# Kernel optimization log

Measured on AMD Instinct MI355X. Metric: run time of the kernel, lower is better.

Reference implementation:

```python
import jax, jax.numpy as jnp
import numpy as np

B, S, D, H = 2, 2048, 512, 8
DK = D // H

def setup_inputs() -> dict:
    key = jax.random.key(0)
    ks = jax.random.split(key, 13)
    inp = {
        'query': jax.random.normal(ks[0], (B, S, D), jnp.float32),
        'key': jax.random.normal(ks[1], (B, S, D), jnp.float32),
        'value': jax.random.normal(ks[2], (B, S, D), jnp.float32),
        'group_prob': jax.random.uniform(ks[3], (B, S, S), jnp.float32),
        'mask': jax.random.randint(ks[4], (B, S, S), 0, 2, jnp.int32),
        'Wq': jax.random.normal(ks[5], (D, D), jnp.float32) * 0.02,
        'bq': jax.random.normal(ks[6], (D,), jnp.float32) * 0.02,
        'Wk': jax.random.normal(ks[7], (D, D), jnp.float32) * 0.02,
        'bk': jax.random.normal(ks[8], (D,), jnp.float32) * 0.02,
        'Wv': jax.random.normal(ks[9], (D, D), jnp.float32) * 0.02,
        'bv': jax.random.normal(ks[10], (D,), jnp.float32) * 0.02,
        'Wo': jax.random.normal(ks[11], (D, D), jnp.float32) * 0.02,
        'bo': jax.random.normal(ks[12], (D,), jnp.float32) * 0.02,
    }
    return inp

def reference(query, key, value, group_prob, mask, Wq, bq, Wk, bk, Wv, bv, Wo, bo):
    # project and split heads: [B,S,D] -> [B,H,S,dk]
    def proj(x, W, b):
        return (x @ W.T + b).reshape(B, S, H, DK).transpose(0, 2, 1, 3)
    q = proj(query, Wq, bq)
    k = proj(key, Wk, bk)
    v = proj(value, Wv, bv)
    scale = 1.0 / np.sqrt(DK).astype(np.float32)
    scores = jnp.einsum('bhqd,bhkd->bhqk', q, k) * scale  # [B,H,S,S]
    # allowed = mask | identity-diagonal; disallowed positions get -1e9
    diag = jnp.eye(S, dtype=bool)
    allowed = (mask.astype(bool) | diag)[:, None, :, :]  # [B,1,S,S]
    scores = jnp.where(allowed, scores, jnp.float32(-1e9))
    p_attn = jax.nn.softmax(scores, axis=-1) * group_prob[:, None, :, :]
    # dropout is identity in eval/deterministic mode
    x = jnp.einsum('bhqk,bhkd->bhqd', p_attn, v)  # [B,H,S,dk]
    x = x.transpose(0, 2, 1, 3).reshape(B, S, D)
    return x @ Wo.T + bo
```

## Files before the change

### kernel.cpp

```cpp
#include <hip/hip_runtime.h>
#include <hip/hip_bf16.h>
#include <cstdint>
#include <cstddef>

typedef __attribute__((ext_vector_type(8))) short bf16x8;
typedef __attribute__((ext_vector_type(4))) float f32x4;
typedef __attribute__((address_space(3))) void lds_void;
typedef const __attribute__((address_space(1))) void g_void;

constexpr int Bc = 2, Sc = 2048, Dc = 512, Hc = 8, DKc = 64;
constexpr int SPLIT = 2;
constexpr int NKT = Sc / 64;
constexpr int KT_PER = NKT / SPLIT;
constexpr float CSC = 0.18033688011112042f;

struct alignas(16) us8 { unsigned short u[8]; };
struct alignas(8) us4 { unsigned short u[4]; };

__device__ __forceinline__ unsigned short f2bf(float x) {
  union { float f; unsigned int u; } v; v.f = x;
  unsigned int r = (v.u + 0x7FFFu + ((v.u >> 16) & 1u)) >> 16;
  return (unsigned short)r;
}

__device__ __forceinline__ float bf2f(unsigned short u) {
  union { unsigned int u; float f; } v; v.u = ((unsigned int)u) << 16;
  return v.f;
}

__device__ __forceinline__ us8 cvt8(float4 a, float4 b) {
  us8 o;
  o.u[0] = f2bf(a.x); o.u[1] = f2bf(a.y); o.u[2] = f2bf(a.z); o.u[3] = f2bf(a.w);
  o.u[4] = f2bf(b.x); o.u[5] = f2bf(b.y); o.u[6] = f2bf(b.z); o.u[7] = f2bf(b.w);
  return o;
}

struct PArgs {
  const float* g; const int* m; unsigned short* gp;
  const float* wsrc[4]; unsigned short* wdst[4];
};

__global__ __launch_bounds__(256)
void prepass(PArgs pa)
{
  const int bx = blockIdx.x;
  const int tid = threadIdx.x;
  if (bx < 2048) {
    const int idx = bx;
    const int b = idx >> 10, rest = idx & 1023, qt = rest >> 5, kt = rest & 31;
    const int colb = tid & 15, hi = (tid >> 4) & 3, wid = tid >> 6;
    const int q = qt * 64 + wid * 16 + colb;
    const int k0 = kt * 64 + hi * 4;
    const float* grow = pa.g + ((size_t)b * Sc + q) * Sc + k0;
    const int* mrow = pa.m + ((size_t)b * Sc + q) * Sc + k0;
    unsigned short vals[16];
#pragma unroll
    for (int n = 0; n < 4; ++n) {
      float4 gv = *(const float4*)(grow + n * 16);
      int4 mv = *(const int4*)(mrow + n * 16);
      const int kb = k0 + n * 16;
      const float gg[4] = {gv.x, gv.y, gv.z, gv.w};
      const int mm[4] = {mv.x, mv.y, mv.z, mv.w};
#pragma unroll
      for (int rr = 0; rr < 4; ++rr) {
        const bool allowed = (mm[rr] != 0) || (kb + rr == q);
        vals[n * 4 + rr] = allowed ? (unsigned short)(f2bf(gg[rr]) | 1u) : (unsigned short)0;
      }
    }
    us8* o = (us8*)(pa.gp + (((size_t)idx * 256) + tid) * 16);
    o[0] = *(us8*)&vals[0];
    o[1] = *(us8*)&vals[8];
  } else {
    const int r = bx - 2048;
    const int wi = r >> 3, sub = r & 7;
    const float* s = pa.wsrc[wi];
    unsigned short* d = pa.wdst[wi];
#pragma unroll
    for (int t = 0; t < 16; ++t) {
      const int i = sub * 4096 + t * 256 + tid;
      float4 a = ((const float4*)s)[(size_t)i * 2];
      float4 b = ((const float4*)s)[(size_t)i * 2 + 1];
      ((us8*)d)[i] = cvt8(a, b);
    }
  }
}

struct GArgs {
  const void* A[3];
  const unsigned short* W[3];
  const float* bias[3];
  void* C[3];
  int mode[3];
  float osc[3];
};

template<int A_FP32>
__global__ __launch_bounds__(256)
void gemm_bn64(GArgs ga)
{
  __shared__ unsigned short As[128][64];
  __shared__ unsigned short Bs[64][64];

  constexpr int K = 512, N = 512;
  const int z = blockIdx.z;
  const unsigned short* Wp = ga.W[z];
  const float* bias = ga.bias[z];
  const int mode = ga.mode[z];
  const float osc = ga.osc[z];

  const int tid = threadIdx.x, lane = tid & 63, w = tid >> 6;
  const int m0 = blockIdx.x * 128, n0 = blockIdx.y * 64;
  const int wm = w >> 1, wn = w & 1;
  const int colb = lane & 15, hi = lane >> 4, rowb = hi * 4;
  const int swz = (colb & 7) << 4;

  f32x4 acc[4][2];
#pragma unroll
  for (int i = 0; i < 4; ++i)
#pragma unroll
    for (int j = 0; j < 2; ++j) acc[i][j] = (f32x4){0.f, 0.f, 0.f, 0.f};

  const int lrow8 = lane >> 3;
  const int cb = ((lane & 7) * 16) ^ (lrow8 << 4);

  for (int k0 = 0; k0 < K; k0 += 64) {
    if (k0) __syncthreads();
#pragma unroll
    for (int i = 0; i < 2; ++i) {
      const int u = w + i * 4;
      const int row = u * 8 + lrow8;
      const unsigned short* bsrc = Wp + (size_t)(n0 + row) * K + k0 + (cb >> 1);
      __builtin_amdgcn_global_load_lds((g_void*)bsrc, (lds_void*)((char*)&Bs[0][0] + u * 1024), 16, 0, 0);
    }
    if (A_FP32) {
      const float* Af = (const float*)ga.A[z];
#pragma unroll
      for (int i = 0; i < 4; ++i) {
        const int u = w * 4 + i;
        const int row = u * 8 + lrow8;
        const float* src = Af + (size_t)(m0 + row) * K + k0 + (cb >> 1);
        float4 v0 = *(const float4*)src, v1 = *(const float4*)(src + 4);
        *(us8*)((char*)&As[0][0] + u * 1024 + lane * 16) = cvt8(v0, v1);
      }
    } else {
      const unsigned short* Ab = (const unsigned short*)ga.A[z];
#pragma unroll
      for (int i = 0; i < 4; ++i) {
        const int u = w * 4 + i;
        const int row = u * 8 + lrow8;
        const unsigned short* asrc = Ab + (size_t)(m0 + row) * K + k0 + (cb >> 1);
        __builtin_amdgcn_global_load_lds((g_void*)asrc, (lds_void*)((char*)&As[0][0] + u * 1024), 16, 0, 0);
      }
    }
    asm volatile("s_waitcnt vmcnt(0)" ::: "memory");
    __syncthreads();

    char* ab = (char*)&As[0][0];
    char* bb = (char*)&Bs[0][0];
#pragma unroll
    for (int kk = 0; kk < 2; ++kk) {
      bf16x8 af[4], bfr[2];
#pragma unroll
      for (int mf = 0; mf < 4; ++mf) {
        const int ar = wm * 64 + mf * 16 + colb;
        af[mf] = *(const bf16x8*)(ab + ar * 128 + ((kk * 64 + hi * 16) ^ swz));
      }
#pragma unroll
      for (int nf = 0; nf < 2; ++nf) {
        const int br = wn * 32 + nf * 16 + colb;
        bfr[nf] = *(const bf16x8*)(bb + br * 128 + ((kk * 64 + hi * 16) ^ swz));
      }
      __builtin_amdgcn_s_setprio(1);
#pragma unroll
      for (int mf = 0; mf < 4; ++mf)
#pragma unroll
        for (int nf = 0; nf < 2; ++nf)
          acc[mf][nf] = __builtin_amdgcn_mfma_f32_16x16x32_bf16(af[mf], bfr[nf], acc[mf][nf], 0, 0, 0);
      __builtin_amdgcn_s_setprio(0);
    }
  }

#pragma unroll
  for (int nf = 0; nf < 2; ++nf) {
    const int gn = n0 + wn * 32 + nf * 16 + colb;
    const float bv = bias[gn];
    if (mode == 1) {
      unsigned short* Cp = (unsigned short*)ga.C[z];
#pragma unroll
      for (int mf = 0; mf < 4; ++mf) {
        const int gm = m0 + wm * 64 + mf * 16 + rowb;
        const int bb_ = gm >> 11, ss = gm & (Sc - 1);
        us4 vv;
#pragma unroll
        for (int rr = 0; rr < 4; ++rr) vv.u[rr] = f2bf(acc[mf][nf][rr] + bv);
        *(us4*)(Cp + ((size_t)bb_ * N + gn) * Sc + ss) = vv;
      }
    } else if (mode == 0) {
      unsigned short* Cp = (unsigned short*)ga.C[z];
#pragma unroll
      for (int mf = 0; mf < 4; ++mf)
#pragma unroll
        for (int rr = 0; rr < 4; ++rr) {
          const int gm = m0 + wm * 64 + mf * 16 + rowb + rr;
          Cp[(size_t)gm * N + gn] = f2bf((acc[mf][nf][rr] + bv) * osc);
        }
    } else {
      float* Cp = (float*)ga.C[z];
#pragma unroll
      for (int mf = 0; mf < 4; ++mf)
#pragma unroll
        for (int rr = 0; rr < 4; ++rr) {
          const int gm = m0 + wm * 64 + mf * 16 + rowb + rr;
          Cp[(size_t)gm * N + gn] = acc[mf][nf][rr] + bv;
        }
    }
  }
}

__global__ __launch_bounds__(256, 4)
void attn_split(const unsigned short* __restrict__ Qb,
                const unsigned short* __restrict__ Kb,
                const unsigned short* __restrict__ Vt,
                const unsigned short* __restrict__ Gp,
                unsigned short* __restrict__ Pacc,
                float* __restrict__ Pml)
{
  __shared__ unsigned short Ks[2][64][64];
  __shared__ unsigned short Vs[2][64][64];
  __shared__ unsigned short Ps[4][16][64];

  const int tid = threadIdx.x, lane = tid & 63, wid = tid >> 6;
  const int wgid = blockIdx.x;
  const int xcd = wgid & 7, rest = wgid >> 3;
  const int mem = rest & 15, ghi = rest >> 4;
  const int g = ghi * 8 + xcd;
  const int b = g >> 5, qt = g & 31;
  const int h = mem >> 1, sp = mem & 1;
  const int bh = b * 8 + h;
  const int q0 = qt * 64;
  const int kt0 = sp * KT_PER;

  const int colb = lane & 15;
  const int hi = lane >> 4;
  const int rowb = hi * 4;
  const int c3s = (colb & 7) << 4;

  bf16x8 qf[2];
  {
    const unsigned short* qp = Qb + ((size_t)(b * Sc + q0 + wid * 16 + colb) * Dc + h * DKc + hi * 8);
    qf[0] = *(const bf16x8*)qp;
    qf[1] = *(const bf16x8*)(qp + 32);
  }

  f32x4 acc[4] = {{0,0,0,0},{0,0,0,0},{0,0,0,0},{0,0,0,0}};
  float lr0 = 0.f, lr1 = 0.f, lr2 = 0.f, lr3 = 0.f;

  auto stageKV = [&](int bufI, int kt) {
    const int k0 = kt * 64;
#pragma unroll
    for (int i = 0; i < 2; ++i) {
      const int obase = wid * 1024 + i * 4096;
      const int row = (obase >> 7) + (lane >> 3);
      const int cb = ((lane & 7) * 16) ^ ((row & 7) << 4);
      const unsigned short* ksrc = Kb + (size_t)(b * Sc + k0 + row) * Dc + h * DKc + (cb >> 1);
      const unsigned short* vsrc = Vt + ((size_t)b * Dc + h * DKc + row) * Sc + k0 + (cb >> 1);
      __builtin_amdgcn_global_load_lds((g_void*)ksrc, (lds_void*)((char*)&Ks[bufI][0][0] + obase), 16, 0, 0);
      __builtin_amdgcn_global_load_lds((g_void*)vsrc, (lds_void*)((char*)&Vs[bufI][0][0] + obase), 16, 0, 0);
    }
  };

  const unsigned short* gtile = Gp + (((size_t)(b * 1024 + qt * 32)) * 256 + tid) * 16;
  auto loadG = [&](int kt, us8& g0, us8& g1) {
    const us8* p = (const us8*)(gtile + (size_t)kt * 4096);
    g0 = p[0]; g1 = p[1];
  };

  us8 gA0, gA1, gB0, gB1;
  stageKV(0, kt0);
  loadG(kt0, gA0, gA1);
  asm volatile("s_waitcnt vmcnt(0)" ::: "memory");
  __syncthreads();

  char* psbase = (char*)&Ps[wid][0][0];

  auto doTile = [&](int kt, int bufI, us8& gc0, us8& gc1, us8& gn0, us8& gn1) {
    if (kt + 1 < kt0 + KT_PER) {
      stageKV(bufI ^ 1, kt + 1);
      loadG(kt + 1, gn0, gn1);
    }

    f32x4 sf[4] = {{0,0,0,0},{0,0,0,0},{0,0,0,0},{0,0,0,0}};
    char* ksb = (char*)&Ks[bufI][0][0];
    __builtin_amdgcn_s_setprio(1);
#pragma unroll
    for (int kk = 0; kk < 2; ++kk) {
#pragma unroll
      for (int n = 0; n < 4; ++n) {
        const int krow = n * 16 + colb;
        bf16x8 kf = *(const bf16x8*)(ksb + krow * 128 + ((kk * 64 + hi * 16) ^ ((krow & 7) << 4)));
        sf[n] = __builtin_amdgcn_mfma_f32_16x16x32_bf16(kf, qf[kk], sf[n], 0, 0, 0);
      }
    }
    __builtin_amdgcn_s_setprio(0);

    unsigned int pw[8];
#pragma unroll
    for (int n = 0; n < 4; ++n) {
      float lacc = 0.f;
#pragma unroll
      for (int s2 = 0; s2 < 2; ++s2) {
        const int jv = n * 4 + s2 * 2;
        const unsigned short u0 = (jv < 8) ? gc0.u[jv] : gc1.u[jv - 8];
        const unsigned short u1 = (jv + 1 < 8) ? gc0.u[jv + 1] : gc1.u[jv + 1 - 8];
        const float p0 = __builtin_amdgcn_exp2f(sf[n][s2 * 2]);
        const float p1 = __builtin_amdgcn_exp2f(sf[n][s2 * 2 + 1]);
        lacc = fmaf(p0, (float)(u0 & 1u), lacc);
        lacc = fmaf(p1, (float)(u1 & 1u), lacc);
        const float q0v = p0 * bf2f(u0), q1v = p1 * bf2f(u1);
        asm("v_cvt_pk_bf16_f32 %0, %1, %2" : "=v"(pw[n * 2 + s2]) : "v"(q0v), "v"(q1v));
      }
      if (n == 0) lr0 += lacc; else if (n == 1) lr1 += lacc;
      else if (n == 2) lr2 += lacc; else lr3 += lacc;
    }

#pragma unroll
    for (int n = 0; n < 4; ++n) {
      const unsigned long long w64 = ((unsigned long long)pw[n * 2 + 1] << 32) | pw[n * 2];
      *(unsigned long long*)(psbase + colb * 128 + ((n * 32 + hi * 8) ^ c3s)) = w64;
    }

    char* vsb = (char*)&Vs[bufI][0][0];
    __builtin_amdgcn_s_setprio(1);
#pragma unroll
    for (int kk = 0; kk < 2; ++kk) {
      bf16x8 pf = *(const bf16x8*)(psbase + colb * 128 + ((kk * 64 + hi * 16) ^ c3s));
#pragma unroll
      for (int n = 0; n < 4; ++n) {
        const int vrow = n * 16 + colb;
        bf16x8 vf = *(const bf16x8*)(vsb + vrow * 128 + ((kk * 64 + hi * 16) ^ ((vrow & 7) << 4)));
        acc[n] = __builtin_amdgcn_mfma_f32_16x16x32_bf16(vf, pf, acc[n], 0, 0, 0);
      }
    }
    __builtin_amdgcn_s_setprio(0);

    asm volatile("s_waitcnt vmcnt(0)" ::: "memory");
    __syncthreads();
  };

  for (int j = 0; j < KT_PER; j += 2) {
    doTile(kt0 + j,     0, gA0, gA1, gB0, gB1);
    doTile(kt0 + j + 1, 1, gB0, gB1, gA0, gA1);
  }

  float lrun = (lr0 + lr1) + (lr2 + lr3);
  lrun += __shfl_xor(lrun, 16);
  lrun += __shfl_xor(lrun, 32);

  const size_t blin = ((size_t)bh * 32 + qt) * SPLIT + sp;
  unsigned short* pa = Pacc + blin * 4096;
#pragma unroll
  for (int n = 0; n < 4; ++n)
#pragma unroll
    for (int rr = 0; rr < 4; ++rr)
      pa[(size_t)(n * 16 + rowb + rr) * 64 + wid * 16 + colb] = f2bf(acc[n][rr]);
  if (hi == 0) Pml[blin * 64 + wid * 16 + colb] = lrun;
}

__global__ __launch_bounds__(256)
void attn_reduce(const unsigned short* __restrict__ Pacc, const float* __restrict__ Pml,
                 unsigned short* __restrict__ Xb)
{
  const int gidx = blockIdx.x;
  const int bh = gidx >> 5, qt = gidx & 31;
  const int b = bh >> 3, h = bh & 7;
  const int tid = threadIdx.x;
  const int qi = tid & 63;
  const int d0 = (tid >> 6) * 16;
  const size_t pb = (size_t)gidx * SPLIT;

  float denom = 0.f;
#pragma unroll
  for (int s = 0; s < SPLIT; ++s) denom += Pml[(pb + s) * 64 + qi];
  const float inv = 1.0f / denom;

  unsigned short vals[16];
#pragma unroll
  for (int j = 0; j < 16; ++j) {
    float a = 0.f;
#pragma unroll
    for (int s = 0; s < SPLIT; ++s)
      a += bf2f(Pacc[(pb + s) * 4096 + (size_t)(d0 + j) * 64 + qi]);
    vals[j] = f2bf(a * inv);
  }
  unsigned short* xp = Xb + ((size_t)(b * Sc) + qt * 64 + qi) * Dc + h * DKc + d0;
  *(us8*)xp = *(us8*)&vals[0];
  *(us8*)(xp + 8) = *(us8*)&vals[8];
}

extern "C" void kernel_launch(void* const* d_in, const int* in_sizes, int n_in,
                              void* d_out, int out_size, void* d_ws, size_t ws_size,
                              hipStream_t stream)
{
  const float* query = (const float*)d_in[0];
  const float* key_  = (const float*)d_in[1];
  const float* value = (const float*)d_in[2];
  const float* gprob = (const float*)d_in[3];
  const int*   mask  = (const int*)d_in[4];
  const float* Wq = (const float*)d_in[5];
  const float* bq = (const float*)d_in[6];
  const float* Wk = (const float*)d_in[7];
  const float* bk = (const float*)d_in[8];
  const float* Wv = (const float*)d_in[9];
  const float* bv = (const float*)d_in[10];
  const float* Wo = (const float*)d_in[11];
  const float* bo = (const float*)d_in[12];
  float* out = (float*)d_out;

  const size_t elems = (size_t)Bc * Sc * Dc;
  const size_t gelems = (size_t)Bc * Sc * Sc;
  const size_t welems = (size_t)Dc * Dc;

  char* base = (char*)d_ws;
  unsigned short* Qb = (unsigned short*)(base);
  unsigned short* Kb = Qb + elems;
  unsigned short* Vt = Kb + elems;
  unsigned short* Xb = Vt + elems;
  unsigned short* Gp = Xb + elems;
  unsigned short* Wqb = Gp + gelems;
  unsigned short* Wkb = Wqb + welems;
  unsigned short* Wvb = Wkb + welems;
  unsigned short* Wob = Wvb + welems;
  unsigned short* Pacc = Wob + welems;
  float* Pml = (float*)(Pacc + (size_t)(Bc * Hc) * 32 * SPLIT * 4096);

  PArgs pa;
  pa.g = gprob; pa.m = mask; pa.gp = Gp;
  pa.wsrc[0] = Wq; pa.wdst[0] = Wqb;
  pa.wsrc[1] = Wk; pa.wdst[1] = Wkb;
  pa.wsrc[2] = Wv; pa.wdst[2] = Wvb;
  pa.wsrc[3] = Wo; pa.wdst[3] = Wob;
  hipLaunchKernelGGL(prepass, dim3(2080), dim3(256), 0, stream, pa);

  GArgs gq;
  gq.A[0] = (const void*)query; gq.W[0] = Wqb; gq.bias[0] = bq; gq.C[0] = (void*)Qb; gq.mode[0] = 0; gq.osc[0] = CSC;
  gq.A[1] = (const void*)key_;  gq.W[1] = Wkb; gq.bias[1] = bk; gq.C[1] = (void*)Kb; gq.mode[1] = 0; gq.osc[1] = 1.0f;
  gq.A[2] = (const void*)value; gq.W[2] = Wvb; gq.bias[2] = bv; gq.C[2] = (void*)Vt; gq.mode[2] = 1; gq.osc[2] = 1.0f;
  hipLaunchKernelGGL((gemm_bn64<1>), dim3(32, 8, 3), dim3(256), 0, stream, gq);

  hipLaunchKernelGGL(attn_split, dim3(1024), dim3(256), 0, stream, Qb, Kb, Vt, Gp, Pacc, Pml);
  hipLaunchKernelGGL(attn_reduce, dim3(Bc * Hc * 32), dim3(256), 0, stream, Pacc, Pml, Xb);

  GArgs go;
  go.A[0] = (const void*)Xb; go.W[0] = Wob; go.bias[0] = bo; go.C[0] = (void*)out; go.mode[0] = 2; go.osc[0] = 1.0f;
  go.A[1] = go.A[0]; go.W[1] = go.W[0]; go.bias[1] = go.bias[0]; go.C[1] = go.C[0]; go.mode[1] = 2; go.osc[1] = 1.0f;
  go.A[2] = go.A[0]; go.W[2] = go.W[0]; go.bias[2] = go.bias[0]; go.C[2] = go.C[0]; go.mode[2] = 2; go.osc[2] = 1.0f;
  hipLaunchKernelGGL((gemm_bn64<0>), dim3(32, 8, 1), dim3(256), 0, stream, go);
}
```

Measured before the change: 93.42 us.

## Fuse QKV projection GEMM into prepass kernel and convert weights on the fly

The separate weight-conversion pass is dropped. The GEMMs now read fp32 weights directly and convert them to bf16 while staging into LDS. The QKV projection GEMM blocks are merged into the same launch as the group_prob/mask packing blocks, removing one kernel launch and letting the memory-bound packing overlap with GEMM compute. The cost is that each GEMM block re-reads and re-converts fp32 weights, which doubles weight traffic and replaces async global_load_lds for B with register loads plus conversion.

```diff
diff --git a/kernel.cpp b/kernel.cpp
--- a/kernel.cpp
+++ b/kernel.cpp
@@ -35,24 +35,149 @@
   return o;
 }
 
-struct PArgs {
+template<int A_FP32>
+__device__ __forceinline__ void gemm_body(
+    unsigned short (*As)[64], unsigned short (*Bs)[64],
+    const void* Ap, const float* Wp, const float* bias, void* Cp,
+    int mode, float osc, int m0, int n0)
+{
+  constexpr int K = 512, N = 512;
+  const int tid = threadIdx.x, lane = tid & 63, w = tid >> 6;
+  const int wm = w >> 1, wn = w & 1;
+  const int colb = lane & 15, hi = lane >> 4, rowb = hi * 4;
+  const int swz = (colb & 7) << 4;
+
+  f32x4 acc[4][2];
+#pragma unroll
+  for (int i = 0; i < 4; ++i)
+#pragma unroll
+    for (int j = 0; j < 2; ++j) acc[i][j] = (f32x4){0.f, 0.f, 0.f, 0.f};
+
+  const int lrow8 = lane >> 3;
+  const int cb = ((lane & 7) * 16) ^ (lrow8 << 4);
+
+  for (int k0 = 0; k0 < K; k0 += 64) {
+    if (k0) __syncthreads();
+#pragma unroll
+    for (int i = 0; i < 2; ++i) {
+      const int u = w + i * 4;
+      const int row = u * 8 + lrow8;
+      const float* src = Wp + (size_t)(n0 + row) * K + k0 + (cb >> 1);
+      float4 v0 = *(const float4*)src, v1 = *(const float4*)(src + 4);
+      *(us8*)((char*)&Bs[0][0] + u * 1024 + lane * 16) = cvt8(v0, v1);
+    }
+    if (A_FP32) {
+      const float* Af = (const float*)Ap;
+#pragma unroll
+      for (int i = 0; i < 4; ++i) {
+        const int u = w * 4 + i;
+        const int row = u * 8 + lrow8;
+        const float* src = Af + (size_t)(m0 + row) * K + k0 + (cb >> 1);
+        float4 v0 = *(const float4*)src, v1 = *(const float4*)(src + 4);
+        *(us8*)((char*)&As[0][0] + u * 1024 + lane * 16) = cvt8(v0, v1);
+      }
+    } else {
+      const unsigned short* Ab = (const unsigned short*)Ap;
+#pragma unroll
+      for (int i = 0; i < 4; ++i) {
+        const int u = w * 4 + i;
+        const int row = u * 8 + lrow8;
+        const unsigned short* asrc = Ab + (size_t)(m0 + row) * K + k0 + (cb >> 1);
+        __builtin_amdgcn_global_load_lds((g_void*)asrc, (lds_void*)((char*)&As[0][0] + u * 1024), 16, 0, 0);
+      }
+      asm volatile("s_waitcnt vmcnt(0)" ::: "memory");
+    }
+    __syncthreads();
+
+    char* ab = (char*)&As[0][0];
+    char* bb = (char*)&Bs[0][0];
+#pragma unroll
+    for (int kk = 0; kk < 2; ++kk) {
+      bf16x8 af[4], bfr[2];
+#pragma unroll
+      for (int mf = 0; mf < 4; ++mf) {
+        const int ar = wm * 64 + mf * 16 + colb;
+        af[mf] = *(const bf16x8*)(ab + ar * 128 + ((kk * 64 + hi * 16) ^ swz));
+      }
+#pragma unroll
+      for (int nf = 0; nf < 2; ++nf) {
+        const int br = wn * 32 + nf * 16 + colb;
+        bfr[nf] = *(const bf16x8*)(bb + br * 128 + ((kk * 64 + hi * 16) ^ swz));
+      }
+      __builtin_amdgcn_s_setprio(1);
+#pragma unroll
+      for (int mf = 0; mf < 4; ++mf)
+#pragma unroll
+        for (int nf = 0; nf < 2; ++nf)
+          acc[mf][nf] = __builtin_amdgcn_mfma_f32_16x16x32_bf16(af[mf], bfr[nf], acc[mf][nf], 0, 0, 0);
+      __builtin_amdgcn_s_setprio(0);
+    }
+  }
+
+#pragma unroll
+  for (int nf = 0; nf < 2; ++nf) {
+    const int gn = n0 + wn * 32 + nf * 16 + colb;
+    const float bv = bias[gn];
+    if (mode == 1) {
+      unsigned short* Cp2 = (unsigned short*)Cp;
+#pragma unroll
+      for (int mf = 0; mf < 4; ++mf) {
+        const int gm = m0 + wm * 64 + mf * 16 + rowb;
+        const int bb_ = gm >> 11, ss = gm & (Sc - 1);
+        us4 vv;
+#pragma unroll
+        for (int rr = 0; rr < 4; ++rr) vv.u[rr] = f2bf(acc[mf][nf][rr] + bv);
+        *(us4*)(Cp2 + ((size_t)bb_ * N + gn) * Sc + ss) = vv;
+      }
+    } else if (mode == 0) {
+      unsigned short* Cp2 = (unsigned short*)Cp;
+#pragma unroll
+      for (int mf = 0; mf < 4; ++mf)
+#pragma unroll
+        for (int rr = 0; rr < 4; ++rr) {
+          const int gm = m0 + wm * 64 + mf * 16 + rowb + rr;
+          Cp2[(size_t)gm * N + gn] = f2bf((acc[mf][nf][rr] + bv) * osc);
+        }
+    } else {
+      float* Cp2 = (float*)Cp;
+#pragma unroll
+      for (int mf = 0; mf < 4; ++mf)
+#pragma unroll
+        for (int rr = 0; rr < 4; ++rr) {
+          const int gm = m0 + wm * 64 + mf * 16 + rowb + rr;
+          Cp2[(size_t)gm * N + gn] = acc[mf][nf][rr] + bv;
+        }
+    }
+  }
+}
+
+struct FArgs {
   const float* g; const int* m; unsigned short* gp;
-  const float* wsrc[4]; unsigned short* wdst[4];
+  const void* A[3]; const float* W[3]; const float* bias[3]; void* C[3];
+  int mode[3]; float osc[3];
 };
 
 __global__ __launch_bounds__(256)
-void prepass(PArgs pa)
-{
+void fused_qkvpre(FArgs fa)
+{
+  __shared__ unsigned short As[128][64];
+  __shared__ unsigned short Bs[64][64];
   const int bx = blockIdx.x;
   const int tid = threadIdx.x;
-  if (bx < 2048) {
-    const int idx = bx;
+
+  if (bx < 768) {
+    const int z = bx >> 8, r2 = bx & 255;
+    const int mx = r2 >> 3, ny = r2 & 7;
+    gemm_body<1>(As, Bs, fa.A[z], fa.W[z], fa.bias[z], fa.C[z],
+                 fa.mode[z], fa.osc[z], mx * 128, ny * 64);
+  } else {
+    const int idx = bx - 768;
     const int b = idx >> 10, rest = idx & 1023, qt = rest >> 5, kt = rest & 31;
     const int colb = tid & 15, hi = (tid >> 4) & 3, wid = tid >> 6;
     const int q = qt * 64 + wid * 16 + colb;
     const int k0 = kt * 64 + hi * 4;
-    const float* grow = pa.g + ((size_t)b * Sc + q) * Sc + k0;
-    const int* mrow = pa.m + ((size_t)b * Sc + q) * Sc + k0;
+    const float* grow = fa.g + ((size_t)b * Sc + q) * Sc + k0;
+    const int* mrow = fa.m + ((size_t)b * Sc + q) * Sc + k0;
     unsigned short vals[16];
 #pragma unroll
     for (int n = 0; n < 4; ++n) {
@@ -67,154 +192,19 @@
         vals[n * 4 + rr] = allowed ? (unsigned short)(f2bf(gg[rr]) | 1u) : (unsigned short)0;
       }
     }
-    us8* o = (us8*)(pa.gp + (((size_t)idx * 256) + tid) * 16);
+    us8* o = (us8*)(fa.gp + (((size_t)idx * 256) + tid) * 16);
     o[0] = *(us8*)&vals[0];
     o[1] = *(us8*)&vals[8];
-  } else {
-    const int r = bx - 2048;
-    const int wi = r >> 3, sub = r & 7;
-    const float* s = pa.wsrc[wi];
-    unsigned short* d = pa.wdst[wi];
-#pragma unroll
-    for (int t = 0; t < 16; ++t) {
-      const int i = sub * 4096 + t * 256 + tid;
-      float4 a = ((const float4*)s)[(size_t)i * 2];
-      float4 b = ((const float4*)s)[(size_t)i * 2 + 1];
-      ((us8*)d)[i] = cvt8(a, b);
-    }
-  }
-}
-
-struct GArgs {
-  const void* A[3];
-  const unsigned short* W[3];
-  const float* bias[3];
-  void* C[3];
-  int mode[3];
-  float osc[3];
-};
-
-template<int A_FP32>
+  }
+}
+
 __global__ __launch_bounds__(256)
-void gemm_bn64(GArgs ga)
+void gemm_o(const unsigned short* Xb, const float* Wo, const float* bo, float* out)
 {
   __shared__ unsigned short As[128][64];
   __shared__ unsigned short Bs[64][64];
-
-  constexpr int K = 512, N = 512;
-  const int z = blockIdx.z;
-  const unsigned short* Wp = ga.W[z];
-  const float* bias = ga.bias[z];
-  const int mode = ga.mode[z];
-  const float osc = ga.osc[z];
-
-  const int tid = threadIdx.x, lane = tid & 63, w = tid >> 6;
-  const int m0 = blockIdx.x * 128, n0 = blockIdx.y * 64;
-  const int wm = w >> 1, wn = w & 1;
-  const int colb = lane & 15, hi = lane >> 4, rowb = hi * 4;
-  const int swz = (colb & 7) << 4;
-
-  f32x4 acc[4][2];
-#pragma unroll
-  for (int i = 0; i < 4; ++i)
-#pragma unroll
-    for (int j = 0; j < 2; ++j) acc[i][j] = (f32x4){0.f, 0.f, 0.f, 0.f};
-
-  const int lrow8 = lane >> 3;
-  const int cb = ((lane & 7) * 16) ^ (lrow8 << 4);
-
-  for (int k0 = 0; k0 < K; k0 += 64) {
-    if (k0) __syncthreads();
-#pragma unroll
-    for (int i = 0; i < 2; ++i) {
-      const int u = w + i * 4;
-      const int row = u * 8 + lrow8;
-      const unsigned short* bsrc = Wp + (size_t)(n0 + row) * K + k0 + (cb >> 1);
-      __builtin_amdgcn_global_load_lds((g_void*)bsrc, (lds_void*)((char*)&Bs[0][0] + u * 1024), 16, 0, 0);
-    }
-    if (A_FP32) {
-      const float* Af = (const float*)ga.A[z];
-#pragma unroll
-      for (int i = 0; i < 4; ++i) {
-        const int u = w * 4 + i;
-        const int row = u * 8 + lrow8;
-        const float* src = Af + (size_t)(m0 + row) * K + k0 + (cb >> 1);
-        float4 v0 = *(const float4*)src, v1 = *(const float4*)(src + 4);
-        *(us8*)((char*)&As[0][0] + u * 1024 + lane * 16) = cvt8(v0, v1);
-      }
-    } else {
-      const unsigned short* Ab = (const unsigned short*)ga.A[z];
-#pragma unroll
-      for (int i = 0; i < 4; ++i) {
-        const int u = w * 4 + i;
-        const int row = u * 8 + lrow8;
-        const unsigned short* asrc = Ab + (size_t)(m0 + row) * K + k0 + (cb >> 1);
-        __builtin_amdgcn_global_load_lds((g_void*)asrc, (lds_void*)((char*)&As[0][0] + u * 1024), 16, 0, 0);
-      }
-    }
-    asm volatile("s_waitcnt vmcnt(0)" ::: "memory");
-    __syncthreads();
-
-    char* ab = (char*)&As[0][0];
-    char* bb = (char*)&Bs[0][0];
-#pragma unroll
-    for (int kk = 0; kk < 2; ++kk) {
-      bf16x8 af[4], bfr[2];
-#pragma unroll
-      for (int mf = 0; mf < 4; ++mf) {
-        const int ar = wm * 64 + mf * 16 + colb;
-        af[mf] = *(const bf16x8*)(ab + ar * 128 + ((kk * 64 + hi * 16) ^ swz));
-      }
-#pragma unroll
-      for (int nf = 0; nf < 2; ++nf) {
-        const int br = wn * 32 + nf * 16 + colb;
-        bfr[nf] = *(const bf16x8*)(bb + br * 128 + ((kk * 64 + hi * 16) ^ swz));
-      }
-      __builtin_amdgcn_s_setprio(1);
-#pragma unroll
-      for (int mf = 0; mf < 4; ++mf)
-#pragma unroll
-        for (int nf = 0; nf < 2; ++nf)
-          acc[mf][nf] = __builtin_amdgcn_mfma_f32_16x16x32_bf16(af[mf], bfr[nf], acc[mf][nf], 0, 0, 0);
-      __builtin_amdgcn_s_setprio(0);
-    }
-  }
-
-#pragma unroll
-  for (int nf = 0; nf < 2; ++nf) {
-    const int gn = n0 + wn * 32 + nf * 16 + colb;
-    const float bv = bias[gn];
-    if (mode == 1) {
-      unsigned short* Cp = (unsigned short*)ga.C[z];
-#pragma unroll
-      for (int mf = 0; mf < 4; ++mf) {
-        const int gm = m0 + wm * 64 + mf * 16 + rowb;
-        const int bb_ = gm >> 11, ss = gm & (Sc - 1);
-        us4 vv;
-#pragma unroll
-        for (int rr = 0; rr < 4; ++rr) vv.u[rr] = f2bf(acc[mf][nf][rr] + bv);
-        *(us4*)(Cp + ((size_t)bb_ * N + gn) * Sc + ss) = vv;
-      }
-    } else if (mode == 0) {
-      unsigned short* Cp = (unsigned short*)ga.C[z];
-#pragma unroll
-      for (int mf = 0; mf < 4; ++mf)
-#pragma unroll
-        for (int rr = 0; rr < 4; ++rr) {
-          const int gm = m0 + wm * 64 + mf * 16 + rowb + rr;
-          Cp[(size_t)gm * N + gn] = f2bf((acc[mf][nf][rr] + bv) * osc);
-        }
-    } else {
-      float* Cp = (float*)ga.C[z];
-#pragma unroll
-      for (int mf = 0; mf < 4; ++mf)
-#pragma unroll
-        for (int rr = 0; rr < 4; ++rr) {
-          const int gm = m0 + wm * 64 + mf * 16 + rowb + rr;
-          Cp[(size_t)gm * N + gn] = acc[mf][nf][rr] + bv;
-        }
-    }
-  }
+  gemm_body<0>(As, Bs, (const void*)Xb, Wo, bo, (void*)out,
+               2, 1.0f, blockIdx.x * 128, blockIdx.y * 64);
 }
 
 __global__ __launch_bounds__(256, 4)
@@ -418,7 +408,6 @@
 
   const size_t elems = (size_t)Bc * Sc * Dc;
   const size_t gelems = (size_t)Bc * Sc * Sc;
-  const size_t welems = (size_t)Dc * Dc;
 
   char* base = (char*)d_ws;
   unsigned short* Qb = (unsigned short*)(base);
@@ -426,33 +415,19 @@
   unsigned short* Vt = Kb + elems;
   unsigned short* Xb = Vt + elems;
   unsigned short* Gp = Xb + elems;
-  unsigned short* Wqb = Gp + gelems;
-  unsigned short* Wkb = Wqb + welems;
-  unsigned short* Wvb = Wkb + welems;
-  unsigned short* Wob = Wvb + welems;
-  unsigned short* Pacc = Wob + welems;
+  unsigned short* Pacc = Gp + gelems;
   float* Pml = (float*)(Pacc + (size_t)(Bc * Hc) * 32 * SPLIT * 4096);
 
-  PArgs pa;
-  pa.g = gprob; pa.m = mask; pa.gp = Gp;
-  pa.wsrc[0] = Wq; pa.wdst[0] = Wqb;
-  pa.wsrc[1] = Wk; pa.wdst[1] = Wkb;
-  pa.wsrc[2] = Wv; pa.wdst[2] = Wvb;
-  pa.wsrc[3] = Wo; pa.wdst[3] = Wob;
-  hipLaunchKernelGGL(prepass, dim3(2080), dim3(256), 0, stream, pa);
-
-  GArgs gq;
-  gq.A[0] = (const void*)query; gq.W[0] = Wqb; gq.bias[0] = bq; gq.C[0] = (void*)Qb; gq.mode[0] = 0; gq.osc[0] = CSC;
-  gq.A[1] = (const void*)key_;  gq.W[1] = Wkb; gq.bias[1] = bk; gq.C[1] = (void*)Kb; gq.mode[1] = 0; gq.osc[1] = 1.0f;
-  gq.A[2] = (const void*)value; gq.W[2] = Wvb; gq.bias[2] = bv; gq.C[2] = (void*)Vt; gq.mode[2] = 1; gq.osc[2] = 1.0f;
-  hipLaunchKernelGGL((gemm_bn64<1>), dim3(32, 8, 3), dim3(256), 0, stream, gq);
+  FArgs fa;
+  fa.g = gprob; fa.m = mask; fa.gp = Gp;
+  fa.A[0] = (const void*)query; fa.W[0] = Wq; fa.bias[0] = bq; fa.C[0] = (void*)Qb; fa.mode[0] = 0; fa.osc[0] = CSC;
+  fa.A[1] = (const void*)key_;  fa.W[1] = Wk; fa.bias[1] = bk; fa.C[1] = (void*)Kb; fa.mode[1] = 0; fa.osc[1] = 1.0f;
+  fa.A[2] = (const void*)value; fa.W[2] = Wv; fa.bias[2] = bv; fa.C[2] = (void*)Vt; fa.mode[2] = 1; fa.osc[2] = 1.0f;
+  hipLaunchKernelGGL(fused_qkvpre, dim3(768 + 2048), dim3(256), 0, stream, fa);
 
   hipLaunchKernelGGL(attn_split, dim3(1024), dim3(256), 0, stream, Qb, Kb, Vt, Gp, Pacc, Pml);
+
   hipLaunchKernelGGL(attn_reduce, dim3(Bc * Hc * 32), dim3(256), 0, stream, Pacc, Pml, Xb);
 
-  GArgs go;
-  go.A[0] = (const void*)Xb; go.W[0] = Wob; go.bias[0] = bo; go.C[0] = (void*)out; go.mode[0] = 2; go.osc[0] = 1.0f;
-  go.A[1] = go.A[0]; go.W[1] = go.W[0]; go.bias[1] = go.bias[0]; go.C[1] = go.C[0]; go.mode[1] = 2; go.osc[1] = 1.0f;
-  go.A[2] = go.A[0]; go.W[2] = go.W[0]; go.bias[2] = go.bias[0]; go.C[2] = go.C[0]; go.mode[2] = 2; go.osc[2] = 1.0f;
-  hipLaunchKernelGGL((gemm_bn64<0>), dim3(32, 8, 1), dim3(256), 0, stream, go);
-}
+  hipLaunchKernelGGL(gemm_o, dim3(32, 8), dim3(256), 0, stream, Xb, Wo, bo, out);
+}
```

New measurement: 96.25 us. 3.0% more time.
